# Performance work log

Hardware: AMD Instinct MI355X
Metric: run time of the kernel (lower is better)

## Reference

```python
import jax, jax.numpy as jnp
import numpy as np

T, B, L, H, IN = 256, 64, 4, 1024, 1024


def setup_inputs() -> dict:
    key = jax.random.key(0)
    k1, k2, k3 = jax.random.split(key, 3)
    x = jax.random.normal(k1, (T, B, IN), dtype=jnp.float32)
    h = jnp.zeros((L, B, H), dtype=jnp.float32)
    # nn.Linear default init: U(-1/sqrt(fan_in), 1/sqrt(fan_in)), fan_in = IN + H
    bound = 1.0 / np.sqrt(IN + H)
    # Stacked per-layer weights: W[l] is [IN+H, 2H] (transposed vs torch), b[l] is [2H]
    W = jax.random.uniform(k2, (L, IN + H, 2 * H), dtype=jnp.float32, minval=-bound, maxval=bound)
    b = jax.random.uniform(k3, (L, 2 * H), dtype=jnp.float32, minval=-bound, maxval=bound)
    return {"x": x, "h": h, "W": W, "b": b}


def reference(x, h, W, b):
    """SRU-cell stacked RNN.
    x: [T, B, IN]; h: [L, B, H]; W: [L, IN+H, 2H]; b: [L, 2H].
    Returns (outputs [T, B, H], h_final [L*B, H]) matching the torch module
    (torch.cat(h, 0) concatenates layer states along the batch axis).
    """
    num_layers = W.shape[0]

    def step(hs, x_t):  # hs: [L, B, H], x_t: [B, IN]
        inp = x_t
        new_hs = []
        for i in range(num_layers):
            z = jnp.concatenate([inp, hs[i]], axis=-1) @ W[i] + b[i]  # [B, 2H]
            learn, forget = jnp.split(z, 2, axis=-1)
            f = jax.nn.sigmoid(forget)
            hn = f * hs[i] + (1.0 - f) * jnp.tanh(learn)  # [B, H]
            new_hs.append(hn)
            inp = hn  # cell output is both next-layer input and new hidden
        return jnp.stack(new_hs), inp

    h_final, outputs = jax.lax.scan(step, h, x)
    return outputs, h_final.reshape(-1, h_final.shape[-1])
```

## Files before the change

### kernel.cpp

```cpp
#include <hip/hip_runtime.h>


typedef _Float16 f16;
typedef _Float16 f16x8 __attribute__((ext_vector_type(8)));
typedef _Float16 f16x4 __attribute__((ext_vector_type(4)));
typedef float    floatx4 __attribute__((ext_vector_type(4)));

#define T_ 256
#define B_ 64
#define L_ 4
#define H_ 1024
#define IN_ 1024
#define K_ 2048

#define RING_ELEMS (B_*H_)
#define RING_BYTES ((size_t)L_*T_*RING_ELEMS*2)
#define CTRL_OFF   RING_BYTES
#define CTRL_BYTES 4096
#define X16_OFF    (CTRL_OFF + 65536)

__global__ void convert_x_kernel(const float* __restrict__ x, f16* __restrict__ x16) {
  const int nvec = (T_*B_*IN_)/4;
  const int stride = gridDim.x*blockDim.x;
  for (int v = blockIdx.x*blockDim.x + threadIdx.x; v < nvec; v += stride) {
    floatx4 in = ((const floatx4*)x)[v];
    f16x4 o; o.x = (f16)in.x; o.y = (f16)in.y; o.z = (f16)in.z; o.w = (f16)in.w;
    ((f16x4*)x16)[v] = o;
  }
}

__device__ __forceinline__ void poll64(const unsigned int* slots, unsigned int tgt) {
  const unsigned int* p = slots + (threadIdx.x & 63);
  for (;;) {
    unsigned int v = __hip_atomic_load(p, __ATOMIC_RELAXED, __HIP_MEMORY_SCOPE_SYSTEM);
    if (__all((int)(v >= tgt))) break;
    __builtin_amdgcn_s_sleep(2);
  }
  asm volatile("" ::: "memory");
}

__device__ __forceinline__ void sc1_store_f16(f16* p, float v) {
  f16 hv = (f16)v;
  unsigned int u = (unsigned int)__builtin_bit_cast(unsigned short, hv);
  asm volatile("global_store_short %0, %1, off sc0 sc1"
               :: "v"((void*)p), "v"(u) : "memory");
}

#define MFMA8(AR0, AR1, BASEJ)                                               \
  _Pragma("unroll")                                                          \
  for (int j = 0; j < 8; ++j) {                                              \
    f16x8 b0 = *(const f16x8*)(bp0 + (BASEJ + j)*32);                        \
    f16x8 b1 = *(const f16x8*)(bp1 + (BASEJ + j)*32);                        \
    f16x8 av0 = __builtin_bit_cast(f16x8, AR0[j]);                           \
    f16x8 av1 = __builtin_bit_cast(f16x8, AR1[j]);                           \
    acc[0][0] = __builtin_amdgcn_mfma_f32_16x16x32_f16(av0, b0, acc[0][0], 0,0,0); \
    acc[0][1] = __builtin_amdgcn_mfma_f32_16x16x32_f16(av0, b1, acc[0][1], 0,0,0); \
    acc[1][0] = __builtin_amdgcn_mfma_f32_16x16x32_f16(av1, b0, acc[1][0], 0,0,0); \
    acc[1][1] = __builtin_amdgcn_mfma_f32_16x16x32_f16(av1, b1, acc[1][1], 0,0,0); \
  }

__global__ __launch_bounds__(512, 2) void sru_main(
    const float* __restrict__ W,
    const float* __restrict__ bias,
    const f16*  __restrict__ x16,
    f16*        __restrict__ ring,
    unsigned int* __restrict__ done,
    float*      __restrict__ out)
{
  __shared__ f16 Wt[32][2056];
  __shared__ float red[3][2][2][2][64][4];

  const int bid  = blockIdx.x;
  const int l    = bid >> 6;
  const int c    = bid & 63;
  const int n0   = c*16;
  const int tid  = threadIdx.x;
  const int lane = tid & 63;
  const int quad = lane >> 4;
  const int lc   = lane & 15;
  const int kq   = tid >> 7;
  const int rh   = (tid >> 6) & 1;

  {
    const int jj = tid & 15;
    const int k0 = tid >> 4;
    const float* Wl = W + (size_t)l*K_*2048;
    for (int i = 0; i < 64; ++i) {
      int k = k0 + i*32;
      Wt[jj][k]      = (f16)Wl[(size_t)k*2048 + n0 + jj];
      Wt[16 + jj][k] = (f16)Wl[(size_t)k*2048 + 1024 + n0 + jj];
    }
  }
  const float bl = bias[l*2048 + n0 + lc];
  const float bf = bias[l*2048 + 1024 + n0 + lc];
  __syncthreads();

  floatx4 hreg0 = 0.f, hreg1 = 0.f;

  const bool useH = (kq >= 2);
  const int  kofs = (kq & 1)*512;

  unsigned int* doneL    = done + ((l*2 + rh) << 6);
  unsigned int* donePrev = (l > 0) ? done + (((l-1)*2 + rh) << 6) : (unsigned int*)0;

  const f16* bp0 = &Wt[lc][kq*512 + quad*8];
  const f16* bp1 = &Wt[16 + lc][kq*512 + quad*8];

  for (int t = 0; t < T_; ++t) {
    if (!useH) {
      if (l > 0) poll64(donePrev, (unsigned)(t+1));
    } else {
      if (t > 0) poll64(doneL, (unsigned)t);
    }

    floatx4 acc[2][2];
    acc[0][0] = 0.f; acc[0][1] = 0.f; acc[1][0] = 0.f; acc[1][1] = 0.f;

    if (!(useH && t == 0)) {
      const f16* Abase;
      if (useH)        Abase = ring + (size_t)(l*T_ + (t-1))*RING_ELEMS;
      else if (l == 0) Abase = x16 + (size_t)t*RING_ELEMS;
      else             Abase = ring + (size_t)((l-1)*T_ + t)*RING_ELEMS;

      const f16* ap0 = Abase + (size_t)(rh*32 + lc)*H_ + kofs + quad*8;
      const f16* ap1 = ap0 + 16*H_;

      floatx4 ar0[8], ar1[8];
      #pragma unroll
      for (int j = 0; j < 8; ++j) {
        ar0[j] = *(const floatx4*)(ap0 + j*32);
        ar1[j] = *(const floatx4*)(ap1 + j*32);
      }
      MFMA8(ar0, ar1, 0);
      #pragma unroll
      for (int j = 0; j < 8; ++j) {
        ar0[j] = *(const floatx4*)(ap0 + 256 + j*32);
        ar1[j] = *(const floatx4*)(ap1 + 256 + j*32);
      }
      MFMA8(ar0, ar1, 8);
    }

    if (kq != 0) {
      const int p = kq - 1;
      *(floatx4*)&red[p][rh][0][0][lane][0] = acc[0][0];
      *(floatx4*)&red[p][rh][0][1][lane][0] = acc[0][1];
      *(floatx4*)&red[p][rh][1][0][lane][0] = acc[1][0];
      *(floatx4*)&red[p][rh][1][1][lane][0] = acc[1][1];
    }
    __syncthreads();

    if (kq == 0) {
      #pragma unroll
      for (int p = 0; p < 3; ++p) {
        acc[0][0] += *(const floatx4*)&red[p][rh][0][0][lane][0];
        acc[0][1] += *(const floatx4*)&red[p][rh][0][1][lane][0];
        acc[1][0] += *(const floatx4*)&red[p][rh][1][0][lane][0];
        acc[1][1] += *(const floatx4*)&red[p][rh][1][1][lane][0];
      }
      f16* ringw = ring + (size_t)(l*T_ + t)*RING_ELEMS;
      #pragma unroll
      for (int mt = 0; mt < 2; ++mt) {
        #pragma unroll
        for (int r = 0; r < 4; ++r) {
          float zl = acc[mt][0][r] + bl;
          float zf = acc[mt][1][r] + bf;
          float fg = 1.0f/(1.0f + __expf(-zf));
          float e2 = __expf(2.0f*zl);
          float th = 1.0f - 2.0f/(e2 + 1.0f);
          float hv = (mt == 0) ? hreg0[r] : hreg1[r];
          float hn = fg*hv + (1.0f - fg)*th;
          if (mt == 0) hreg0[r] = hn; else hreg1[r] = hn;
          int row = rh*32 + mt*16 + quad*4 + r;
          int idx = row*H_ + n0 + lc;
          sc1_store_f16(&ringw[idx], hn);
          if (l == 3)      out[(size_t)t*RING_ELEMS + idx] = hn;
          if (t == T_ - 1) out[(size_t)T_*RING_ELEMS + (size_t)l*RING_ELEMS + idx] = hn;
        }
      }
      asm volatile("s_waitcnt vmcnt(0)" ::: "memory");
      if (lane == 0)
        __hip_atomic_store(doneL + c, (unsigned)(t+1),
                           __ATOMIC_RELAXED, __HIP_MEMORY_SCOPE_SYSTEM);
    }
    __syncthreads();
  }
}

extern "C" void kernel_launch(void* const* d_in, const int* in_sizes, int n_in,
                              void* d_out, int out_size, void* d_ws, size_t ws_size,
                              hipStream_t stream) {
  (void)in_sizes; (void)n_in; (void)out_size; (void)ws_size;
  const float* x = (const float*)d_in[0];
  const float* W = (const float*)d_in[2];
  const float* b = (const float*)d_in[3];
  float* out = (float*)d_out;

  char* ws = (char*)d_ws;
  f16* ring = (f16*)ws;
  unsigned int* done = (unsigned int*)(ws + CTRL_OFF);
  f16* x16 = (f16*)(ws + X16_OFF);

  hipMemsetAsync(ws + CTRL_OFF, 0, CTRL_BYTES, stream);
  convert_x_kernel<<<1024, 256, 0, stream>>>(x, x16);

  void* args[] = { (void*)&W, (void*)&b, (void*)&x16, (void*)&ring, (void*)&done, (void*)&out };
  hipLaunchCooperativeKernel((const void*)sru_main, dim3(256), dim3(512), args, 0, stream);
}
```

Before: 3.136 ms.

## Restructure SRU wave split into 16-row groups with finer flags and packed stores

New measurement: 3.452 ms. 10.1% more time.

```diff
diff --git a/kernel.cpp b/kernel.cpp
--- a/kernel.cpp
+++ b/kernel.cpp
@@ -13,8 +13,8 @@
 #define IN_ 1024
 #define K_ 2048
 
-#define RING_ELEMS (B_*H_)
-#define RING_BYTES ((size_t)L_*T_*RING_ELEMS*2)
+#define PANEL (B_*H_)
+#define RING_BYTES ((size_t)L_*T_*PANEL*2)
 #define CTRL_OFF   RING_BYTES
 #define CTRL_BYTES 4096
 #define X16_OFF    (CTRL_OFF + 65536)
@@ -29,35 +29,21 @@
   }
 }
 
-__device__ __forceinline__ void poll64(const unsigned int* slots, unsigned int tgt) {
-  const unsigned int* p = slots + (threadIdx.x & 63);
+__device__ __forceinline__ unsigned poll_line(const unsigned int* line, unsigned tgt) {
+  const unsigned int* p = line + (threadIdx.x & 63);
   for (;;) {
-    unsigned int v = __hip_atomic_load(p, __ATOMIC_RELAXED, __HIP_MEMORY_SCOPE_SYSTEM);
-    if (__all((int)(v >= tgt))) break;
+    unsigned v = __hip_atomic_load(p, __ATOMIC_RELAXED, __HIP_MEMORY_SCOPE_SYSTEM);
+    if (__all((int)(v >= tgt))) {
+      unsigned a = tgt;
+      if      (__all((int)(v >= tgt + 16))) a = tgt + 16;
+      else if (__all((int)(v >= tgt + 4)))  a = tgt + 4;
+      else if (__all((int)(v >= tgt + 1)))  a = tgt + 1;
+      asm volatile("" ::: "memory");
+      return a;
+    }
     __builtin_amdgcn_s_sleep(2);
   }
-  asm volatile("" ::: "memory");
-}
-
-__device__ __forceinline__ void sc1_store_f16(f16* p, float v) {
-  f16 hv = (f16)v;
-  unsigned int u = (unsigned int)__builtin_bit_cast(unsigned short, hv);
-  asm volatile("global_store_short %0, %1, off sc0 sc1"
-               :: "v"((void*)p), "v"(u) : "memory");
-}
-
-#define MFMA8(AR0, AR1, BASEJ)                                               \
-  _Pragma("unroll")                                                          \
-  for (int j = 0; j < 8; ++j) {                                              \
-    f16x8 b0 = *(const f16x8*)(bp0 + (BASEJ + j)*32);                        \
-    f16x8 b1 = *(const f16x8*)(bp1 + (BASEJ + j)*32);                        \
-    f16x8 av0 = __builtin_bit_cast(f16x8, AR0[j]);                           \
-    f16x8 av1 = __builtin_bit_cast(f16x8, AR1[j]);                           \
-    acc[0][0] = __builtin_amdgcn_mfma_f32_16x16x32_f16(av0, b0, acc[0][0], 0,0,0); \
-    acc[0][1] = __builtin_amdgcn_mfma_f32_16x16x32_f16(av0, b1, acc[0][1], 0,0,0); \
-    acc[1][0] = __builtin_amdgcn_mfma_f32_16x16x32_f16(av1, b0, acc[1][0], 0,0,0); \
-    acc[1][1] = __builtin_amdgcn_mfma_f32_16x16x32_f16(av1, b1, acc[1][1], 0,0,0); \
-  }
+}
 
 __global__ __launch_bounds__(512, 2) void sru_main(
     const float* __restrict__ W,
@@ -68,7 +54,8 @@
     float*      __restrict__ out)
 {
   __shared__ f16 Wt[32][2056];
-  __shared__ float red[3][2][2][2][64][4];
+  __shared__ float red[2][4][2][64][4];
+  __shared__ f16 hst[64][24];
 
   const int bid  = blockIdx.x;
   const int l    = bid >> 6;
@@ -78,8 +65,12 @@
   const int lane = tid & 63;
   const int quad = lane >> 4;
   const int lc   = lane & 15;
-  const int kq   = tid >> 7;
-  const int rh   = (tid >> 6) & 1;
+  const int w    = tid >> 6;
+  const int kh   = w & 1;
+  const int mh   = (w >> 1) & 1;
+  const int rh   = w >> 2;
+  const int R    = rh*32 + mh*16;
+  const int grp  = rh*2 + mh;
 
   {
     const int jj = tid & 15;
@@ -95,94 +86,101 @@
   const float bf = bias[l*2048 + 1024 + n0 + lc];
   __syncthreads();
 
-  floatx4 hreg0 = 0.f, hreg1 = 0.f;
-
-  const bool useH = (kq >= 2);
-  const int  kofs = (kq & 1)*512;
-
-  unsigned int* doneL    = done + ((l*2 + rh) << 6);
-  unsigned int* donePrev = (l > 0) ? done + (((l-1)*2 + rh) << 6) : (unsigned int*)0;
-
-  const f16* bp0 = &Wt[lc][kq*512 + quad*8];
-  const f16* bp1 = &Wt[16 + lc][kq*512 + quad*8];
+  floatx4 hreg = 0.f;
+
+  unsigned int* lineL = done + ((l*4 + grp) << 6);
+  unsigned int* lineP = (l > 0) ? done + (((l-1)*4 + grp) << 6) : (unsigned int*)0;
+  unsigned avail = 0;
+
+  const f16* bpL = &Wt[lc][kh*1024 + quad*8];
+  const f16* bpF = &Wt[16 + lc][kh*1024 + quad*8];
 
   for (int t = 0; t < T_; ++t) {
-    if (!useH) {
-      if (l > 0) poll64(donePrev, (unsigned)(t+1));
+    if (kh == 0) {
+      if (l > 0 && avail < (unsigned)(t+1)) avail = poll_line(lineP, (unsigned)(t+1));
     } else {
-      if (t > 0) poll64(doneL, (unsigned)t);
-    }
-
-    floatx4 acc[2][2];
-    acc[0][0] = 0.f; acc[0][1] = 0.f; acc[1][0] = 0.f; acc[1][1] = 0.f;
-
-    if (!(useH && t == 0)) {
+      if (t > 0) poll_line(lineL, (unsigned)t);
+    }
+
+    floatx4 accLa = 0.f, accLb = 0.f, accFa = 0.f, accFb = 0.f;
+
+    if (!(kh == 1 && t == 0)) {
       const f16* Abase;
-      if (useH)        Abase = ring + (size_t)(l*T_ + (t-1))*RING_ELEMS;
-      else if (l == 0) Abase = x16 + (size_t)t*RING_ELEMS;
-      else             Abase = ring + (size_t)((l-1)*T_ + t)*RING_ELEMS;
-
-      const f16* ap0 = Abase + (size_t)(rh*32 + lc)*H_ + kofs + quad*8;
-      const f16* ap1 = ap0 + 16*H_;
-
-      floatx4 ar0[8], ar1[8];
+      if (kh == 1)      Abase = ring + (size_t)(l*T_ + (t-1))*PANEL;
+      else if (l == 0)  Abase = x16 + (size_t)t*PANEL;
+      else              Abase = ring + (size_t)((l-1)*T_ + t)*PANEL;
+      const f16* ap = Abase + (size_t)(R + lc)*H_ + quad*8;
+
       #pragma unroll
-      for (int j = 0; j < 8; ++j) {
-        ar0[j] = *(const floatx4*)(ap0 + j*32);
-        ar1[j] = *(const floatx4*)(ap1 + j*32);
-      }
-      MFMA8(ar0, ar1, 0);
+      for (int g = 0; g < 4; ++g) {
+        floatx4 ar[8];
+        #pragma unroll
+        for (int j = 0; j < 8; ++j)
+          ar[j] = *(const floatx4*)(ap + (g*8 + j)*32);
+        #pragma unroll
+        for (int j = 0; j < 8; ++j) {
+          f16x8 av = __builtin_bit_cast(f16x8, ar[j]);
+          f16x8 bL = *(const f16x8*)(bpL + (g*8 + j)*32);
+          f16x8 bF = *(const f16x8*)(bpF + (g*8 + j)*32);
+          if (g & 1) {
+            accLb = __builtin_amdgcn_mfma_f32_16x16x32_f16(av, bL, accLb, 0,0,0);
+            accFb = __builtin_amdgcn_mfma_f32_16x16x32_f16(av, bF, accFb, 0,0,0);
+          } else {
+            accLa = __builtin_amdgcn_mfma_f32_16x16x32_f16(av, bL, accLa, 0,0,0);
+            accFa = __builtin_amdgcn_mfma_f32_16x16x32_f16(av, bF, accFa, 0,0,0);
+          }
+        }
+      }
+    }
+
+    if (kh == 1) {
+      *(floatx4*)&red[t&1][grp][0][lane][0] = accLa + accLb;
+      *(floatx4*)&red[t&1][grp][1][lane][0] = accFa + accFb;
+    }
+    __syncthreads();
+
+    if (kh == 0) {
+      floatx4 zL = accLa + accLb + *(const floatx4*)&red[t&1][grp][0][lane][0];
+      floatx4 zF = accFa + accFb + *(const floatx4*)&red[t&1][grp][1][lane][0];
+      f16* ringw = ring + (size_t)(l*T_ + t)*PANEL;
+
       #pragma unroll
-      for (int j = 0; j < 8; ++j) {
-        ar0[j] = *(const floatx4*)(ap0 + 256 + j*32);
-        ar1[j] = *(const floatx4*)(ap1 + 256 + j*32);
-      }
-      MFMA8(ar0, ar1, 8);
-    }
-
-    if (kq != 0) {
-      const int p = kq - 1;
-      *(floatx4*)&red[p][rh][0][0][lane][0] = acc[0][0];
-      *(floatx4*)&red[p][rh][0][1][lane][0] = acc[0][1];
-      *(floatx4*)&red[p][rh][1][0][lane][0] = acc[1][0];
-      *(floatx4*)&red[p][rh][1][1][lane][0] = acc[1][1];
-    }
-    __syncthreads();
-
-    if (kq == 0) {
-      #pragma unroll
-      for (int p = 0; p < 3; ++p) {
-        acc[0][0] += *(const floatx4*)&red[p][rh][0][0][lane][0];
-        acc[0][1] += *(const floatx4*)&red[p][rh][0][1][lane][0];
-        acc[1][0] += *(const floatx4*)&red[p][rh][1][0][lane][0];
-        acc[1][1] += *(const floatx4*)&red[p][rh][1][1][lane][0];
-      }
-      f16* ringw = ring + (size_t)(l*T_ + t)*RING_ELEMS;
-      #pragma unroll
-      for (int mt = 0; mt < 2; ++mt) {
-        #pragma unroll
-        for (int r = 0; r < 4; ++r) {
-          float zl = acc[mt][0][r] + bl;
-          float zf = acc[mt][1][r] + bf;
-          float fg = 1.0f/(1.0f + __expf(-zf));
-          float e2 = __expf(2.0f*zl);
-          float th = 1.0f - 2.0f/(e2 + 1.0f);
-          float hv = (mt == 0) ? hreg0[r] : hreg1[r];
-          float hn = fg*hv + (1.0f - fg)*th;
-          if (mt == 0) hreg0[r] = hn; else hreg1[r] = hn;
-          int row = rh*32 + mt*16 + quad*4 + r;
-          int idx = row*H_ + n0 + lc;
-          sc1_store_f16(&ringw[idx], hn);
-          if (l == 3)      out[(size_t)t*RING_ELEMS + idx] = hn;
-          if (t == T_ - 1) out[(size_t)T_*RING_ELEMS + (size_t)l*RING_ELEMS + idx] = hn;
-        }
+      for (int r = 0; r < 4; ++r) {
+        float zl = zL[r] + bl;
+        float zf = zF[r] + bf;
+        float fg = 1.0f/(1.0f + __expf(-zf));
+        float th = 1.0f - 2.0f/(__expf(2.0f*zl) + 1.0f);
+        float hn = fg*hreg[r] + (1.0f - fg)*th;
+        hreg[r] = hn;
+        hst[R + quad*4 + r][lc] = (f16)hn;
+      }
+      asm volatile("s_waitcnt lgkmcnt(0)" ::: "memory");
+      __builtin_amdgcn_sched_barrier(0);
+
+      if (lane < 32) {
+        int srow = R + (lane >> 1);
+        int sh   = lane & 1;
+        floatx4 hv = *(const floatx4*)&hst[srow][sh*8];
+        asm volatile("global_store_dwordx4 %0, %1, off sc0 sc1"
+                     :: "v"((void*)(ringw + (size_t)srow*H_ + n0 + sh*8)),
+                        "v"(hv) : "memory");
       }
       asm volatile("s_waitcnt vmcnt(0)" ::: "memory");
       if (lane == 0)
-        __hip_atomic_store(doneL + c, (unsigned)(t+1),
+        __hip_atomic_store(lineL + c, (unsigned)(t+1),
                            __ATOMIC_RELAXED, __HIP_MEMORY_SCOPE_SYSTEM);
-    }
-    __syncthreads();
+
+      if (l == 3) {
+        #pragma unroll
+        for (int r = 0; r < 4; ++r)
+          out[(size_t)t*PANEL + (size_t)(R + quad*4 + r)*H_ + n0 + lc] = hreg[r];
+      }
+      if (t == T_ - 1) {
+        #pragma unroll
+        for (int r = 0; r < 4; ++r)
+          out[(size_t)T_*PANEL + (size_t)l*PANEL + (size_t)(R + quad*4 + r)*H_ + n0 + lc] = hreg[r];
+      }
+    }
   }
 }
 
```
